# Optimization experiments

Hardware: AMD Instinct MI355X
Metric: run time of the kernel (lower is better)

The kernel has to match this reference:

```python
import jax, jax.numpy as jnp
import numpy as np

DIM = 1024
HEADS = 16
HIDDEN = 4096
EPS = 1e-5

def setup_inputs() -> dict:
    key = jax.random.key(0)
    ks = jax.random.split(key, 8)
    s = 0.02
    return {
        "x": jax.random.normal(ks[0], (4, 1024, DIM), dtype=jnp.float32),
        "ln1_g": jnp.ones((DIM,), jnp.float32),
        "ln1_b": jnp.zeros((DIM,), jnp.float32),
        "w_qkv": jax.random.normal(ks[1], (DIM, 3 * DIM), jnp.float32) * s,
        "b_qkv": jnp.zeros((3 * DIM,), jnp.float32),
        "w_proj": jax.random.normal(ks[2], (DIM, DIM), jnp.float32) * s,
        "b_proj": jnp.zeros((DIM,), jnp.float32),
        "ln2_g": jnp.ones((DIM,), jnp.float32),
        "ln2_b": jnp.zeros((DIM,), jnp.float32),
        "w_fc1": jax.random.normal(ks[3], (DIM, HIDDEN), jnp.float32) * s,
        "b_fc1": jnp.zeros((HIDDEN,), jnp.float32),
        "w_fc2": jax.random.normal(ks[4], (HIDDEN, DIM), jnp.float32) * s,
        "b_fc2": jnp.zeros((DIM,), jnp.float32),
    }

def _layernorm(x, g, b):
    mu = jnp.mean(x, axis=-1, keepdims=True)
    var = jnp.mean(jnp.square(x - mu), axis=-1, keepdims=True)
    return (x - mu) * jax.lax.rsqrt(var + EPS) * g + b

def _block(x, ln1_g, ln1_b, w_qkv, b_qkv, w_proj, b_proj,
           ln2_g, ln2_b, w_fc1, b_fc1, w_fc2, b_fc2):
    B, N, C = x.shape
    H = HEADS
    Dh = C // H
    scale = Dh ** -0.5
    # --- attention branch (pre-norm) ---
    h = _layernorm(x, ln1_g, ln1_b)
    qkv = h @ w_qkv + b_qkv                       # [B,N,3C]
    qkv = qkv.reshape(B, N, 3, H, Dh)
    q, k, v = qkv[:, :, 0], qkv[:, :, 1], qkv[:, :, 2]  # [B,N,H,Dh]
    attn = jnp.einsum("bnhd,bmhd->bhnm", q, k) * scale  # [B,H,N,N]
    attn = jax.nn.softmax(attn, axis=-1)
    o = jnp.einsum("bhnm,bmhd->bnhd", attn, v).reshape(B, N, C)
    x = x + (o @ w_proj + b_proj)
    # --- MLP branch (pre-norm) ---
    h = _layernorm(x, ln2_g, ln2_b)
    h = jax.nn.gelu(h @ w_fc1 + b_fc1, approximate=False)
    x = x + (h @ w_fc2 + b_fc2)
    return x

def reference(x, ln1_g, ln1_b, w_qkv, b_qkv, w_proj, b_proj,
              ln2_g, ln2_b, w_fc1, b_fc1, w_fc2, b_fc2):
    return _block(x, ln1_g, ln1_b, w_qkv, b_qkv, w_proj, b_proj,
                  ln2_g, ln2_b, w_fc1, b_fc1, w_fc2, b_fc2)
```

## Files before the change

### kernel.cpp

```cpp
#include <hip/hip_runtime.h>
#include <hip/hip_bf16.h>

typedef __attribute__((ext_vector_type(8))) short bf16x8;
typedef __attribute__((ext_vector_type(4))) float f32x4;

__device__ __forceinline__ ushort f2bf(float f) {
  unsigned int u = __float_as_uint(f);
  u += 0x7fffu + ((u >> 16) & 1u);
  return (ushort)(u >> 16);
}

__device__ __forceinline__ void gl_lds16(const void* g, void* l) {
  __builtin_amdgcn_global_load_lds(
      (const __attribute__((address_space(1))) void*)g,
      (__attribute__((address_space(3))) void*)l, 16, 0, 0);
}

__global__ __launch_bounds__(256) void transpose_w(
    const float* __restrict__ W, ushort* __restrict__ Wt, int K, int N) {
  __shared__ float tile[32][33];
  const int tx = threadIdx.x, ty = threadIdx.y;
  const int bx = blockIdx.x, by = blockIdx.y;
#pragma unroll
  for (int j = 0; j < 4; j++)
    tile[ty + j * 8][tx] = W[(size_t)(by * 32 + ty + j * 8) * N + bx * 32 + tx];
  __syncthreads();
#pragma unroll
  for (int j = 0; j < 4; j++)
    Wt[(size_t)(bx * 32 + ty + j * 8) * K + by * 32 + tx] =
        f2bf(tile[tx][ty + j * 8]);
}

__global__ __launch_bounds__(256) void transpose_v(
    const ushort* __restrict__ qkv, ushort* __restrict__ vt) {
  __shared__ ushort tile[32][33];
  const int tx = threadIdx.x, ty = threadIdx.y;
  const int n0 = blockIdx.x * 32;
  const int d0 = blockIdx.y * 32;
  const int bh = blockIdx.z;
  const int bidx = bh >> 4, h = bh & 15;
#pragma unroll
  for (int j = 0; j < 4; j++)
    tile[ty + j * 8][tx] =
        qkv[(size_t)(bidx * 1024 + n0 + ty + j * 8) * 3072 + 2048 + h * 64 +
            d0 + tx];
  __syncthreads();
#pragma unroll
  for (int j = 0; j < 4; j++)
    vt[(size_t)(bh * 64 + d0 + ty + j * 8) * 1024 + n0 + tx] =
        tile[tx][ty + j * 8];
}

__global__ __launch_bounds__(256) void ln_bf16(
    const float* __restrict__ x, const float* __restrict__ g,
    const float* __restrict__ b, ushort* __restrict__ out) {
  const int row = blockIdx.x;
  const int t = threadIdx.x;
  float4 v = ((const float4*)(x + (size_t)row * 1024))[t];
  float s = v.x + v.y + v.z + v.w;
  float ss = v.x * v.x + v.y * v.y + v.z * v.z + v.w * v.w;
#pragma unroll
  for (int msk = 1; msk < 64; msk <<= 1) {
    s += __shfl_xor(s, msk);
    ss += __shfl_xor(ss, msk);
  }
  __shared__ float red[8];
  const int wv = t >> 6, ln = t & 63;
  if (ln == 0) { red[wv * 2] = s; red[wv * 2 + 1] = ss; }
  __syncthreads();
  s = red[0] + red[2] + red[4] + red[6];
  ss = red[1] + red[3] + red[5] + red[7];
  const float mu = s * (1.0f / 1024.0f);
  const float var = ss * (1.0f / 1024.0f) - mu * mu;
  const float rstd = rsqrtf(var + 1e-5f);
  float4 gv = ((const float4*)g)[t];
  float4 bv = ((const float4*)b)[t];
  ushort4 o;
  o.x = f2bf((v.x - mu) * rstd * gv.x + bv.x);
  o.y = f2bf((v.y - mu) * rstd * gv.y + bv.y);
  o.z = f2bf((v.z - mu) * rstd * gv.z + bv.z);
  o.w = f2bf((v.w - mu) * rstd * gv.w + bv.w);
  ((ushort4*)(out + (size_t)row * 1024))[t] = o;
}

template <int BM, int BN, int NW, int OCC, int EPI>
__global__ __launch_bounds__(NW * 64, OCC) void gemm32(
    const ushort* __restrict__ A, const ushort* __restrict__ Bt,
    const float* __restrict__ bias, const float* __restrict__ resid,
    void* __restrict__ outp, int M, int N, int K, int cw, int ch, int xw) {
  constexpr int WN = NW / 2;
  constexpr int BWN = BN / WN;
  constexpr int MF = BM / 2 / 16;
  constexpr int NF = BWN / 16;
  constexpr int CA = BM / 64, CB = BN / 64;
  __shared__ ushort smem[2 * (BM + BN) * 32];
  const int t = threadIdx.x;
  const int lane = t & 63, wid = t >> 6;
  const int lr = lane & 15, lc = lane >> 4;
  const int wr = wid / WN, wc = wid % WN;

  const int flat = blockIdx.y * gridDim.x + blockIdx.x;
  const int xcd = flat & 7, li = flat >> 3;
  const int bx = (xcd % xw) * cw + (li % cw);
  const int by = (xcd / xw) * ch + (li / cw);
  const int m0 = by * BM, n0 = bx * BN;
  const int nkt = K >> 5;

  const int uoff = ((t & 3) ^ ((t >> 3) & 3)) * 8;
  const int au = (lc ^ ((lr >> 1) & 3)) * 8;

  f32x4 acc[MF][NF];
#pragma unroll
  for (int m = 0; m < MF; m++)
#pragma unroll
    for (int n = 0; n < NF; n++) acc[m][n] = (f32x4){0.f, 0.f, 0.f, 0.f};

  auto stage = [&](int bb, int kt) {
#pragma unroll
    for (int c = 0; c < CA; c++)
      gl_lds16(A + (size_t)(m0 + c * 64 + (t >> 2)) * K + (size_t)(kt * 32) +
                   uoff,
               &smem[bb * BM * 32 + c * 2048 + wid * 512]);
#pragma unroll
    for (int c = 0; c < CB; c++)
      gl_lds16(Bt + (size_t)(n0 + c * 64 + (t >> 2)) * K + (size_t)(kt * 32) +
                   uoff,
               &smem[2 * BM * 32 + bb * BN * 32 + c * 2048 + wid * 512]);
  };
  auto rdA = [&](int bb, int mf) {
    return *(const bf16x8*)&smem[bb * BM * 32 +
                                 (wr * (BM / 2) + mf * 16 + lr) * 32 + au];
  };
  auto rdB = [&](int bb, int nf) {
    return *(const bf16x8*)&smem[2 * BM * 32 + bb * BN * 32 +
                                 (wc * BWN + nf * 16 + lr) * 32 + au];
  };

  stage(0, 0);
  __syncthreads();

  int b = 0;
  for (int kt = 0; kt < nkt; kt++, b ^= 1) {
    if (kt + 1 < nkt) stage(b ^ 1, kt + 1);

    bf16x8 Br[NF];
#pragma unroll
    for (int nf = 0; nf < NF; nf++) Br[nf] = rdB(b, nf);
    bf16x8 Ar[MF];
#pragma unroll
    for (int mf = 0; mf < MF; mf++) Ar[mf] = rdA(b, mf);
#pragma unroll
    for (int mf = 0; mf < MF; mf++)
#pragma unroll
      for (int nf = 0; nf < NF; nf++)
        acc[mf][nf] = __builtin_amdgcn_mfma_f32_16x16x32_bf16(
            Ar[mf], Br[nf], acc[mf][nf], 0, 0, 0);

    __syncthreads();
  }

#pragma unroll
  for (int mf = 0; mf < MF; mf++) {
#pragma unroll
    for (int nf = 0; nf < NF; nf++) {
      const int gr0 = m0 + wr * (BM / 2) + mf * 16 + lc * 4;
      const int gc = n0 + wc * BWN + nf * 16 + lr;
      const float bs = bias[gc];
#pragma unroll
      for (int r = 0; r < 4; r++) {
        const float v = acc[mf][nf][r] + bs;
        const int gr = gr0 + r;
        if (EPI == 0) {
          ((ushort*)outp)[(size_t)gr * N + gc] = f2bf(v);
        } else if (EPI == 1) {
          const float gg = 0.5f * v * (1.0f + erff(v * 0.70710678118654752f));
          ((ushort*)outp)[(size_t)gr * N + gc] = f2bf(gg);
        } else {
          ((float*)outp)[(size_t)gr * N + gc] =
              v + resid[(size_t)gr * N + gc];
        }
      }
    }
  }
}

template <int BM, int BN, int NW, int EPI>
__global__ __launch_bounds__(NW * 64, 2) void gemm64(
    const ushort* __restrict__ A, const ushort* __restrict__ Bt,
    const float* __restrict__ bias, const float* __restrict__ resid,
    void* __restrict__ outp, int M, int N, int K, int cw, int ch, int xw) {
  constexpr int T = NW * 64;
  constexpr int WN = NW / 2;
  constexpr int BWN = BN / WN;
  constexpr int MF = BM / 2 / 16;
  constexpr int NF = BWN / 16;
  constexpr int CA = BM / 64, CB = BN / 64;
  constexpr int REP = 512 / T;
  __shared__ ushort smem[2 * (BM + BN) * 64];
  const int t = threadIdx.x;
  const int lane = t & 63, wid = t >> 6;
  const int lr = lane & 15, lc = lane >> 4;
  const int wr = wid / WN, wc = wid % WN;

  const int flat = blockIdx.y * gridDim.x + blockIdx.x;
  const int xcd = flat & 7, li = flat >> 3;
  const int bx = (xcd % xw) * cw + (li % cw);
  const int by = (xcd / xw) * ch + (li / cw);
  const int m0 = by * BM, n0 = bx * BN;
  const int nkt = K >> 6;

  const int uoff = ((t & 7) ^ ((t >> 3) & 7)) * 8;
  const int sx = lr & 7;
  const int au0 = (lc ^ sx) * 8;
  const int au1 = ((lc | 4) ^ sx) * 8;

  f32x4 acc[MF][NF];
#pragma unroll
  for (int m = 0; m < MF; m++)
#pragma unroll
    for (int n = 0; n < NF; n++) acc[m][n] = (f32x4){0.f, 0.f, 0.f, 0.f};

  auto stage = [&](int bb, int kt) {
#pragma unroll
    for (int c = 0; c < CA; c++)
#pragma unroll
      for (int r = 0; r < REP; r++)
        gl_lds16(A + (size_t)(m0 + c * 64 + ((r * T + t) >> 3)) * K +
                     (size_t)(kt * 64) + uoff,
                 &smem[bb * BM * 64 + c * 4096 + (r * T + wid * 64) * 8]);
#pragma unroll
    for (int c = 0; c < CB; c++)
#pragma unroll
      for (int r = 0; r < REP; r++)
        gl_lds16(Bt + (size_t)(n0 + c * 64 + ((r * T + t) >> 3)) * K +
                     (size_t)(kt * 64) + uoff,
                 &smem[2 * BM * 64 + bb * BN * 64 + c * 4096 +
                       (r * T + wid * 64) * 8]);
  };
  auto rdA = [&](int bb, int mf, int kk) {
    return *(const bf16x8*)&smem[bb * BM * 64 +
                                 (wr * (BM / 2) + mf * 16 + lr) * 64 +
                                 (kk ? au1 : au0)];
  };
  auto rdB = [&](int bb, int nf, int kk) {
    return *(const bf16x8*)&smem[2 * BM * 64 + bb * BN * 64 +
                                 (wc * BWN + nf * 16 + lr) * 64 +
                                 (kk ? au1 : au0)];
  };

  stage(0, 0);
  __syncthreads();

  int b = 0;
  for (int kt = 0; kt < nkt; kt++, b ^= 1) {
    if (kt + 1 < nkt) stage(b ^ 1, kt + 1);

    bf16x8 Br[NF][2];
#pragma unroll
    for (int nf = 0; nf < NF; nf++) {
      Br[nf][0] = rdB(b, nf, 0);
      Br[nf][1] = rdB(b, nf, 1);
    }
#pragma unroll
    for (int mh = 0; mh < MF / 4; mh++) {
      bf16x8 Ar[4][2];
#pragma unroll
      for (int mf = 0; mf < 4; mf++) {
        Ar[mf][0] = rdA(b, mh * 4 + mf, 0);
        Ar[mf][1] = rdA(b, mh * 4 + mf, 1);
      }
#pragma unroll
      for (int mf = 0; mf < 4; mf++)
#pragma unroll
        for (int nf = 0; nf < NF; nf++) {
          acc[mh * 4 + mf][nf] = __builtin_amdgcn_mfma_f32_16x16x32_bf16(
              Ar[mf][0], Br[nf][0], acc[mh * 4 + mf][nf], 0, 0, 0);
          acc[mh * 4 + mf][nf] = __builtin_amdgcn_mfma_f32_16x16x32_bf16(
              Ar[mf][1], Br[nf][1], acc[mh * 4 + mf][nf], 0, 0, 0);
        }
    }

    __syncthreads();
  }

#pragma unroll
  for (int mf = 0; mf < MF; mf++) {
#pragma unroll
    for (int nf = 0; nf < NF; nf++) {
      const int gr0 = m0 + wr * (BM / 2) + mf * 16 + lc * 4;
      const int gc = n0 + wc * BWN + nf * 16 + lr;
      const float bs = bias[gc];
#pragma unroll
      for (int r = 0; r < 4; r++) {
        const float v = acc[mf][nf][r] + bs;
        const int gr = gr0 + r;
        if (EPI == 0) {
          ((ushort*)outp)[(size_t)gr * N + gc] = f2bf(v);
        } else if (EPI == 1) {
          const float gg = 0.5f * v * (1.0f + erff(v * 0.70710678118654752f));
          ((ushort*)outp)[(size_t)gr * N + gc] = f2bf(gg);
        } else {
          ((float*)outp)[(size_t)gr * N + gc] =
              v + resid[(size_t)gr * N + gc];
        }
      }
    }
  }
}

__global__ __launch_bounds__(256) void attn_kernel(
    const ushort* __restrict__ qkv, const ushort* __restrict__ vt,
    ushort* __restrict__ o_out) {
  __shared__ ushort sK[4096];
  __shared__ ushort sV[4096];
  __shared__ ushort sP[4 * 32 * 72];
  const int t = threadIdx.x;
  const int lane = t & 63, wid = t >> 6;
  const int lr = lane & 15, lc = lane >> 4;
  const int qb = blockIdx.x;
  const int bh = blockIdx.y;
  const int bidx = bh >> 4, h = bh & 15;
  const size_t base = (size_t)bidx * 1024 * 3072;
  const int q0w = qb * 128 + wid * 32;

  bf16x8 qf[2][2];
#pragma unroll
  for (int nf = 0; nf < 2; nf++)
#pragma unroll
    for (int kd = 0; kd < 2; kd++)
      qf[nf][kd] = *(const bf16x8*)&qkv[base +
          (size_t)(q0w + nf * 16 + lr) * 3072 + h * 64 + kd * 32 + lc * 8];

  f32x4 oacc[4][2];
#pragma unroll
  for (int mf = 0; mf < 4; mf++)
#pragma unroll
    for (int nf = 0; nf < 2; nf++) oacc[mf][nf] = (f32x4){0.f, 0.f, 0.f, 0.f};
  float m_r[2] = {-1e30f, -1e30f};
  float l_r[2] = {0.f, 0.f};

  const int srow = lane >> 2;
  const int scol = (lane & 3) * 8;
  ushort* pw = sP + wid * 2304;

  for (int kv0 = 0; kv0 < 1024; kv0 += 64) {
    __syncthreads();
#pragma unroll
    for (int s = 0; s < 2; s++) {
      gl_lds16(qkv + base + (size_t)(kv0 + wid * 16 + srow) * 3072 + 1024 +
                   h * 64 + s * 32 + scol,
               sK + s * 2048 + wid * 512);
      gl_lds16(vt + (size_t)(bh * 64 + wid * 16 + srow) * 1024 + kv0 + s * 32 +
                   scol,
               sV + s * 2048 + wid * 512);
    }
    __syncthreads();

    f32x4 st[4][2];
#pragma unroll
    for (int mf = 0; mf < 4; mf++) {
      bf16x8 ka0 = *(const bf16x8*)&sK[(mf * 16 + lr) * 32 + lc * 8];
      bf16x8 ka1 = *(const bf16x8*)&sK[2048 + (mf * 16 + lr) * 32 + lc * 8];
#pragma unroll
      for (int nf = 0; nf < 2; nf++) {
        f32x4 z = (f32x4){0.f, 0.f, 0.f, 0.f};
        z = __builtin_amdgcn_mfma_f32_16x16x32_bf16(ka0, qf[nf][0], z, 0, 0, 0);
        z = __builtin_amdgcn_mfma_f32_16x16x32_bf16(ka1, qf[nf][1], z, 0, 0, 0);
        st[mf][nf] = z;
      }
    }

#pragma unroll
    for (int nf = 0; nf < 2; nf++) {
      float mx = st[0][nf][0];
#pragma unroll
      for (int mf = 0; mf < 4; mf++)
        mx = fmaxf(mx, fmaxf(fmaxf(st[mf][nf][0], st[mf][nf][1]),
                             fmaxf(st[mf][nf][2], st[mf][nf][3])));
      mx = fmaxf(mx, __shfl_xor(mx, 16));
      mx = fmaxf(mx, __shfl_xor(mx, 32));
      mx *= 0.125f;
      const float mn = fmaxf(m_r[nf], mx);
      const float alpha = __expf(m_r[nf] - mn);
      m_r[nf] = mn;
      float rs = 0.f;
#pragma unroll
      for (int mf = 0; mf < 4; mf++) {
        const float p0 = __expf(fmaf(st[mf][nf][0], 0.125f, -mn));
        const float p1 = __expf(fmaf(st[mf][nf][1], 0.125f, -mn));
        const float p2 = __expf(fmaf(st[mf][nf][2], 0.125f, -mn));
        const float p3 = __expf(fmaf(st[mf][nf][3], 0.125f, -mn));
        rs += (p0 + p1) + (p2 + p3);
        uint2 u;
        u.x = (uint)f2bf(p0) | ((uint)f2bf(p1) << 16);
        u.y = (uint)f2bf(p2) | ((uint)f2bf(p3) << 16);
        *(uint2*)&pw[(nf * 16 + lr) * 72 + mf * 16 + lc * 4] = u;
      }
      rs += __shfl_xor(rs, 16);
      rs += __shfl_xor(rs, 32);
      l_r[nf] = l_r[nf] * alpha + rs;
#pragma unroll
      for (int mf = 0; mf < 4; mf++) {
        oacc[mf][nf][0] *= alpha;
        oacc[mf][nf][1] *= alpha;
        oacc[mf][nf][2] *= alpha;
        oacc[mf][nf][3] *= alpha;
      }
    }

#pragma unroll
    for (int ks = 0; ks < 2; ks++) {
      bf16x8 pb0 = *(const bf16x8*)&pw[lr * 72 + ks * 32 + lc * 8];
      bf16x8 pb1 = *(const bf16x8*)&pw[(16 + lr) * 72 + ks * 32 + lc * 8];
#pragma unroll
      for (int mf = 0; mf < 4; mf++) {
        bf16x8 va = *(const bf16x8*)&sV[ks * 2048 + (mf * 16 + lr) * 32 + lc * 8];
        oacc[mf][0] =
            __builtin_amdgcn_mfma_f32_16x16x32_bf16(va, pb0, oacc[mf][0], 0, 0, 0);
        oacc[mf][1] =
            __builtin_amdgcn_mfma_f32_16x16x32_bf16(va, pb1, oacc[mf][1], 0, 0, 0);
      }
    }
  }

  const float inv[2] = {1.f / l_r[0], 1.f / l_r[1]};
#pragma unroll
  for (int mf = 0; mf < 4; mf++)
#pragma unroll
    for (int nf = 0; nf < 2; nf++) {
      ushort4 o4;
      o4.x = f2bf(oacc[mf][nf][0] * inv[nf]);
      o4.y = f2bf(oacc[mf][nf][1] * inv[nf]);
      o4.z = f2bf(oacc[mf][nf][2] * inv[nf]);
      o4.w = f2bf(oacc[mf][nf][3] * inv[nf]);
      *(ushort4*)&o_out[(size_t)(bidx * 1024 + q0w + nf * 16 + lr) * 1024 +
                        h * 64 + mf * 16 + lc * 4] = o4;
    }
}

extern "C" void kernel_launch(void* const* d_in, const int* in_sizes, int n_in,
                              void* d_out, int out_size, void* d_ws,
                              size_t ws_size, hipStream_t stream) {
  const float* x      = (const float*)d_in[0];
  const float* ln1_g  = (const float*)d_in[1];
  const float* ln1_b  = (const float*)d_in[2];
  const float* w_qkv  = (const float*)d_in[3];
  const float* b_qkv  = (const float*)d_in[4];
  const float* w_proj = (const float*)d_in[5];
  const float* b_proj = (const float*)d_in[6];
  const float* ln2_g  = (const float*)d_in[7];
  const float* ln2_b  = (const float*)d_in[8];
  const float* w_fc1  = (const float*)d_in[9];
  const float* b_fc1  = (const float*)d_in[10];
  const float* w_fc2  = (const float*)d_in[11];
  const float* b_fc2  = (const float*)d_in[12];
  float* out = (float*)d_out;

  ushort* ws      = (ushort*)d_ws;
  ushort* wt_qkv  = ws;
  ushort* wt_proj = wt_qkv + 3072 * 1024;
  ushort* wt_fc1  = wt_proj + 1024 * 1024;
  ushort* wt_fc2  = wt_fc1 + 4096 * 1024;
  ushort* hbuf    = wt_fc2 + 1024 * 4096;
  ushort* qkv     = hbuf + 4096 * 1024;
  ushort* obuf    = qkv + 4096 * 3072;
  ushort* h3      = qkv;
  ushort* vtb     = hbuf;

  transpose_w<<<dim3(96, 32), dim3(32, 8), 0, stream>>>(w_qkv, wt_qkv, 1024, 3072);
  transpose_w<<<dim3(32, 32), dim3(32, 8), 0, stream>>>(w_proj, wt_proj, 1024, 1024);
  transpose_w<<<dim3(128, 32), dim3(32, 8), 0, stream>>>(w_fc1, wt_fc1, 1024, 4096);
  transpose_w<<<dim3(32, 128), dim3(32, 8), 0, stream>>>(w_fc2, wt_fc2, 4096, 1024);

  ln_bf16<<<4096, 256, 0, stream>>>(x, ln1_g, ln1_b, hbuf);
  gemm32<128, 128, 4, 4, 0><<<dim3(24, 32), 256, 0, stream>>>(
      hbuf, wt_qkv, b_qkv, nullptr, qkv, 4096, 3072, 1024, 12, 8, 2);
  transpose_v<<<dim3(32, 2, 64), dim3(32, 8), 0, stream>>>(qkv, vtb);
  attn_kernel<<<dim3(8, 64), 256, 0, stream>>>(qkv, vtb, obuf);
  gemm64<128, 64, 4, 2><<<dim3(16, 32), 256, 0, stream>>>(
      obuf, wt_proj, b_proj, x, out, 4096, 1024, 1024, 8, 8, 2);
  ln_bf16<<<4096, 256, 0, stream>>>(out, ln2_g, ln2_b, hbuf);
  gemm32<128, 128, 4, 4, 1><<<dim3(32, 32), 256, 0, stream>>>(
      hbuf, wt_fc1, b_fc1, nullptr, h3, 4096, 4096, 1024, 16, 8, 2);
  gemm64<128, 64, 4, 2><<<dim3(16, 32), 256, 0, stream>>>(
      h3, wt_fc2, b_fc2, out, out, 4096, 1024, 4096, 8, 8, 2);
}
```

Before: 231.1 us.

## Add 256x256 eight-wave ping-pong GEMM kernel for the FC1 GELU layer

Adds a new bf16 MFMA GEMM with 256x256 tiles, 512 threads and a 128 KB LDS double buffer. Global-to-LDS loads are interleaved with MFMA clusters, separated by barriers, and MFMA issue priority is raised with setprio. The fused GELU FC1 GEMM now uses this kernel instead of the 128x128 gemm32. Larger tiles cut operand reloads, but the grid shrinks to 256 blocks, and the many barriers plus 128 KB of LDS may limit occupancy and tail efficiency.

```diff
diff --git a/kernel.cpp b/kernel.cpp
--- a/kernel.cpp
+++ b/kernel.cpp
@@ -15,6 +15,8 @@
       (const __attribute__((address_space(1))) void*)g,
       (__attribute__((address_space(3))) void*)l, 16, 0, 0);
 }
+
+#define CFENCE() asm volatile("" ::: "memory")
 
 __global__ __launch_bounds__(256) void transpose_w(
     const float* __restrict__ W, ushort* __restrict__ Wt, int K, int N) {
@@ -83,6 +85,171 @@
   ((ushort4*)(out + (size_t)row * 1024))[t] = o;
 }
 
+__device__ __forceinline__ void mma16(f32x4 (&acc)[8][4], bf16x8 (&Ar)[4][2],
+                                      bf16x8 (&Br)[2][2], int mh, int nh) {
+#pragma unroll
+  for (int mf = 0; mf < 4; mf++)
+#pragma unroll
+    for (int nf = 0; nf < 2; nf++) {
+      acc[mh * 4 + mf][nh * 2 + nf] = __builtin_amdgcn_mfma_f32_16x16x32_bf16(
+          Ar[mf][0], Br[nf][0], acc[mh * 4 + mf][nh * 2 + nf], 0, 0, 0);
+      acc[mh * 4 + mf][nh * 2 + nf] = __builtin_amdgcn_mfma_f32_16x16x32_bf16(
+          Ar[mf][1], Br[nf][1], acc[mh * 4 + mf][nh * 2 + nf], 0, 0, 0);
+    }
+}
+
+template <int EPI>
+__global__ __launch_bounds__(512, 2) void gemm8p(
+    const ushort* __restrict__ A, const ushort* __restrict__ Bt,
+    const float* __restrict__ bias, void* __restrict__ outp,
+    int M, int N, int K, int cw, int ch, int xw) {
+  __shared__ ushort smem[65536];
+  const int t = threadIdx.x;
+  const int lane = t & 63, wid = t >> 6;
+  const int lr = lane & 15, lc = lane >> 4;
+  const int wr = wid >> 2, wc = wid & 3;
+
+  const int flat = blockIdx.y * gridDim.x + blockIdx.x;
+  const int xcd = flat & 7, li = flat >> 3;
+  const int bx = (xcd % xw) * cw + (li % cw);
+  const int by = (xcd / xw) * ch + (li / cw);
+  const int m0 = by * 256, n0 = bx * 256;
+  const int nkt = K >> 6;
+  const int niter = nkt >> 1;
+
+  const int sx = lr & 7;
+  const int au0 = (lc ^ sx) * 8;
+  const int au1 = ((lc | 4) ^ sx) * 8;
+
+  f32x4 acc[8][4];
+#pragma unroll
+  for (int m = 0; m < 8; m++)
+#pragma unroll
+    for (int n = 0; n < 4; n++) acc[m][n] = (f32x4){0.f, 0.f, 0.f, 0.f};
+
+  auto stageh = [&](int isB, int bb, int h, int kt) {
+    const ushort* src = isB ? Bt : A;
+    const int base0 = isB ? n0 : m0;
+    const int lds0 = isB * 32768 + (bb * 2 + h) * 8192;
+#pragma unroll
+    for (int r = 0; r < 2; r++) {
+      const int s = r * 512 + t;
+      gl_lds16(src + (size_t)(base0 + h * 128 + (s >> 3)) * K +
+                   (size_t)(kt * 64) + (size_t)(((s & 7) ^ ((s >> 3) & 7)) * 8),
+               &smem[lds0 + s * 8]);
+    }
+  };
+  auto rdA = [&](int bb, int mf, int kk) {
+    return *(const bf16x8*)&smem[(bb * 2 + wr) * 8192 + (mf * 16 + lr) * 64 +
+                                 (kk ? au1 : au0)];
+  };
+  auto rdB = [&](int bb, int nf, int kk) {
+    return *(const bf16x8*)&smem[32768 + (bb * 2 + (wc >> 1)) * 8192 +
+                                 ((wc & 1) * 64 + nf * 16 + lr) * 64 +
+                                 (kk ? au1 : au0)];
+  };
+
+  stageh(0, 0, 0, 0); stageh(0, 0, 1, 0);
+  stageh(1, 0, 0, 0); stageh(1, 0, 1, 0);
+  stageh(0, 1, 0, (nkt > 1) ? 1 : 0);
+  asm volatile("s_waitcnt vmcnt(2)" ::: "memory");
+  __builtin_amdgcn_s_barrier(); CFENCE();
+
+  for (int k = 0; k < niter; k++) {
+    const int odd = 2 * k + 1;
+    const int ne = (2 * k + 2 < nkt) ? 2 * k + 2 : nkt - 1;
+    const int no = (2 * k + 3 < nkt) ? 2 * k + 3 : nkt - 1;
+    bf16x8 Ar[4][2], Br[2][2];
+
+#pragma unroll
+    for (int mf = 0; mf < 4; mf++) { Ar[mf][0] = rdA(0, mf, 0); Ar[mf][1] = rdA(0, mf, 1); }
+    Br[0][0] = rdB(0, 0, 0); Br[0][1] = rdB(0, 0, 1);
+    Br[1][0] = rdB(0, 1, 0); Br[1][1] = rdB(0, 1, 1);
+    stageh(0, 1, 1, odd);
+    __builtin_amdgcn_s_barrier(); CFENCE();
+    __builtin_amdgcn_s_setprio(1); mma16(acc, Ar, Br, 0, 0); __builtin_amdgcn_s_setprio(0);
+    __builtin_amdgcn_s_barrier(); CFENCE();
+
+    Br[0][0] = rdB(0, 2, 0); Br[0][1] = rdB(0, 2, 1);
+    Br[1][0] = rdB(0, 3, 0); Br[1][1] = rdB(0, 3, 1);
+    stageh(1, 1, 0, odd);
+    __builtin_amdgcn_s_barrier(); CFENCE();
+    __builtin_amdgcn_s_setprio(1); mma16(acc, Ar, Br, 0, 1); __builtin_amdgcn_s_setprio(0);
+    __builtin_amdgcn_s_barrier(); CFENCE();
+
+#pragma unroll
+    for (int mf = 0; mf < 4; mf++) { Ar[mf][0] = rdA(0, mf + 4, 0); Ar[mf][1] = rdA(0, mf + 4, 1); }
+    Br[0][0] = rdB(0, 0, 0); Br[0][1] = rdB(0, 0, 1);
+    Br[1][0] = rdB(0, 1, 0); Br[1][1] = rdB(0, 1, 1);
+    stageh(1, 1, 1, odd);
+    __builtin_amdgcn_s_barrier(); CFENCE();
+    __builtin_amdgcn_s_setprio(1); mma16(acc, Ar, Br, 1, 0); __builtin_amdgcn_s_setprio(0);
+    __builtin_amdgcn_s_barrier(); CFENCE();
+
+    Br[0][0] = rdB(0, 2, 0); Br[0][1] = rdB(0, 2, 1);
+    Br[1][0] = rdB(0, 3, 0); Br[1][1] = rdB(0, 3, 1);
+    stageh(0, 0, 0, ne);
+    __builtin_amdgcn_s_barrier(); CFENCE();
+    __builtin_amdgcn_s_setprio(1); mma16(acc, Ar, Br, 1, 1); __builtin_amdgcn_s_setprio(0);
+    asm volatile("s_waitcnt vmcnt(2)" ::: "memory");
+    __builtin_amdgcn_s_barrier(); CFENCE();
+
+#pragma unroll
+    for (int mf = 0; mf < 4; mf++) { Ar[mf][0] = rdA(1, mf, 0); Ar[mf][1] = rdA(1, mf, 1); }
+    Br[0][0] = rdB(1, 0, 0); Br[0][1] = rdB(1, 0, 1);
+    Br[1][0] = rdB(1, 1, 0); Br[1][1] = rdB(1, 1, 1);
+    stageh(0, 0, 1, ne);
+    __builtin_amdgcn_s_barrier(); CFENCE();
+    __builtin_amdgcn_s_setprio(1); mma16(acc, Ar, Br, 0, 0); __builtin_amdgcn_s_setprio(0);
+    __builtin_amdgcn_s_barrier(); CFENCE();
+
+    Br[0][0] = rdB(1, 2, 0); Br[0][1] = rdB(1, 2, 1);
+    Br[1][0] = rdB(1, 3, 0); Br[1][1] = rdB(1, 3, 1);
+    stageh(1, 0, 0, ne);
+    __builtin_amdgcn_s_barrier(); CFENCE();
+    __builtin_amdgcn_s_setprio(1); mma16(acc, Ar, Br, 0, 1); __builtin_amdgcn_s_setprio(0);
+    __builtin_amdgcn_s_barrier(); CFENCE();
+
+#pragma unroll
+    for (int mf = 0; mf < 4; mf++) { Ar[mf][0] = rdA(1, mf + 4, 0); Ar[mf][1] = rdA(1, mf + 4, 1); }
+    Br[0][0] = rdB(1, 0, 0); Br[0][1] = rdB(1, 0, 1);
+    Br[1][0] = rdB(1, 1, 0); Br[1][1] = rdB(1, 1, 1);
+    stageh(1, 0, 1, ne);
+    __builtin_amdgcn_s_barrier(); CFENCE();
+    __builtin_amdgcn_s_setprio(1); mma16(acc, Ar, Br, 1, 0); __builtin_amdgcn_s_setprio(0);
+    __builtin_amdgcn_s_barrier(); CFENCE();
+
+    Br[0][0] = rdB(1, 2, 0); Br[0][1] = rdB(1, 2, 1);
+    Br[1][0] = rdB(1, 3, 0); Br[1][1] = rdB(1, 3, 1);
+    stageh(0, 1, 0, no);
+    __builtin_amdgcn_s_barrier(); CFENCE();
+    __builtin_amdgcn_s_setprio(1); mma16(acc, Ar, Br, 1, 1); __builtin_amdgcn_s_setprio(0);
+    asm volatile("s_waitcnt vmcnt(2)" ::: "memory");
+    __builtin_amdgcn_s_barrier(); CFENCE();
+  }
+
+#pragma unroll
+  for (int mf = 0; mf < 8; mf++) {
+#pragma unroll
+    for (int nf = 0; nf < 4; nf++) {
+      const int gr0 = m0 + wr * 128 + mf * 16 + lc * 4;
+      const int gc = n0 + wc * 64 + nf * 16 + lr;
+      const float bs = bias[gc];
+#pragma unroll
+      for (int r = 0; r < 4; r++) {
+        const float v = acc[mf][nf][r] + bs;
+        const int gr = gr0 + r;
+        if (EPI == 0) {
+          ((ushort*)outp)[(size_t)gr * N + gc] = f2bf(v);
+        } else {
+          const float gg = 0.5f * v * (1.0f + erff(v * 0.70710678118654752f));
+          ((ushort*)outp)[(size_t)gr * N + gc] = f2bf(gg);
+        }
+      }
+    }
+  }
+}
+
 template <int BM, int BN, int NW, int OCC, int EPI>
 __global__ __launch_bounds__(NW * 64, OCC) void gemm32(
     const ushort* __restrict__ A, const ushort* __restrict__ Bt,
@@ -480,8 +647,8 @@
   gemm64<128, 64, 4, 2><<<dim3(16, 32), 256, 0, stream>>>(
       obuf, wt_proj, b_proj, x, out, 4096, 1024, 1024, 8, 8, 2);
   ln_bf16<<<4096, 256, 0, stream>>>(out, ln2_g, ln2_b, hbuf);
-  gemm32<128, 128, 4, 4, 1><<<dim3(32, 32), 256, 0, stream>>>(
-      hbuf, wt_fc1, b_fc1, nullptr, h3, 4096, 4096, 1024, 16, 8, 2);
+  gemm8p<1><<<dim3(16, 16), 512, 0, stream>>>(
+      hbuf, wt_fc1, b_fc1, h3, 4096, 4096, 1024, 4, 8, 4);
   gemm64<128, 64, 4, 2><<<dim3(16, 32), 256, 0, stream>>>(
       h3, wt_fc2, b_fc2, out, out, 4096, 1024, 4096, 8, 8, 2);
 }
```

Result: slower. 241.5 us (+4.5%).
